# Performance work log

Measured on AMD Instinct MI355X. Metric: run time of the kernel, lower is better.

Reference implementation:

```python
import jax, jax.numpy as jnp
import numpy as np

B, S, E, A = 4, 2048, 1024, 64  # batch, seq, embedding_size, attention_size


def setup_inputs() -> dict:
    key = jax.random.key(0)
    k1, k2 = jax.random.split(key)
    embedding = jax.random.normal(k1, (B, S, E), dtype=jnp.float32)
    # nn.Linear(embedding_size, attention_size, bias=False).weight has shape [A, E]
    Wk = jax.random.normal(k2, (A, E), dtype=jnp.float32) * (1.0 / np.sqrt(E))
    return {"embedding": embedding, "Wk": Wk}


def reference(embedding, Wk):
    # NOTE: the original module (buggily) calls self.key() for q, k, AND v.
    # We reproduce that math faithfully: q = k = v = embedding @ Wk.T.
    k = jnp.einsum('bse,ae->bsa', embedding, Wk)  # [B,S,A]
    q = k
    v = k
    x = jnp.einsum('bqa,bka->bqk', q, k) / jnp.sqrt(jnp.float32(A))  # [B,S,S]
    # Faithful to masked_fill(torch.tril(x) == 0, -inf): masks the strict upper
    # triangle (tril zeros it) plus any lower-triangle entries exactly equal to 0.
    x = jnp.where(jnp.tril(x) == 0, -jnp.inf, x)
    x = jax.nn.softmax(x, axis=2)
    return jnp.einsum('bqk,bka->bqa', x, v)  # [B,S,A]
```

## Files before the change

kernel.cpp:

```cpp
#include <hip/hip_runtime.h>
#include <math.h>

#define BATCH 4
#define SLEN  2048
#define EMB   1024
#define AH    64

typedef __attribute__((ext_vector_type(8))) short bf16x8;
typedef __attribute__((ext_vector_type(4))) float f32x4;

#define MFMA16(a, b, c) __builtin_amdgcn_mfma_f32_16x16x32_bf16((a), (b), (c), 0, 0, 0)

__device__ __forceinline__ void async16(const void* g, void* l) {
  __builtin_amdgcn_global_load_lds(
      (const __attribute__((address_space(1))) unsigned int*)g,
      (__attribute__((address_space(3))) unsigned int*)l, 16, 0, 0);
}

__device__ __forceinline__ short f2bf(float x) {
  union { float f; unsigned u; } v; v.f = x;
  unsigned r = v.u + 0x7fffu + ((v.u >> 16) & 1u);
  return (short)(r >> 16);
}
__device__ __forceinline__ float bf2f(short h) {
  union { unsigned u; float f; } v; v.u = ((unsigned)(unsigned short)h) << 16;
  return v.f;
}

__device__ __forceinline__ void split_trunc(float4 a0, float4 a1, bf16x8& hi, bf16x8& lo) {
  unsigned c[8] = {__float_as_uint(a0.x), __float_as_uint(a0.y), __float_as_uint(a0.z),
                   __float_as_uint(a0.w), __float_as_uint(a1.x), __float_as_uint(a1.y),
                   __float_as_uint(a1.z), __float_as_uint(a1.w)};
  union { bf16x8 v; unsigned d[4]; } H, L;
  H.d[0] = __builtin_amdgcn_perm(c[1], c[0], 0x07060302u);
  H.d[1] = __builtin_amdgcn_perm(c[3], c[2], 0x07060302u);
  H.d[2] = __builtin_amdgcn_perm(c[5], c[4], 0x07060302u);
  H.d[3] = __builtin_amdgcn_perm(c[7], c[6], 0x07060302u);
  unsigned e[8];
#pragma unroll
  for (int j = 0; j < 8; ++j)
    e[j] = __float_as_uint(__uint_as_float(c[j]) - __uint_as_float(c[j] & 0xffff0000u));
  L.d[0] = __builtin_amdgcn_perm(e[1], e[0], 0x07060302u);
  L.d[1] = __builtin_amdgcn_perm(e[3], e[2], 0x07060302u);
  L.d[2] = __builtin_amdgcn_perm(e[5], e[4], 0x07060302u);
  L.d[3] = __builtin_amdgcn_perm(e[7], e[6], 0x07060302u);
  hi = H.v; lo = L.v;
}

__device__ __forceinline__ int slot_off(int qt) {
  return (qt == 0) ? 0 : qt + (((qt - 1) * (qt - 1)) >> 2);
}

#define CH_SHORTS 24576


__global__ __launch_bounds__(256) void prep_wk_kernel(const float* __restrict__ Wk,
                                                      short* __restrict__ BpkG) {
  int tg = blockIdx.x * 256 + threadIdx.x;
  int kc = tg >> 8, rem = tg & 255, nt = rem >> 6, lane = rem & 63;
  int n = nt * 16 + (lane & 15);
  int k = kc * 32 + (lane >> 4) * 8;
  const float* src = Wk + (size_t)n * EMB + k;
  float4 a0 = *(const float4*)src;
  float4 a1 = *(const float4*)(src + 4);
  bf16x8 hi, lo;
  split_trunc(a0, a1, hi, lo);
  short* dst = BpkG + ((size_t)(kc * 4 + nt) * 128 + lane) * 8;
  *(bf16x8*)dst = hi;
  *(bf16x8*)(dst + 512) = lo;
}

__global__ __launch_bounds__(256) void gemm_k_kernel(const float* __restrict__ emb,
                                                     const short* __restrict__ BpkG,
                                                     short* __restrict__ Kpack) {
  __shared__ __align__(16) float eT[16384];

  const int t = threadIdx.x;
  const int w = t >> 6, l = t & 63, lm = l & 15, quad = l >> 4;
  const int nt = w;
  const int row0 = blockIdx.x * 16;

  {
    int rowl = 4 * w + (l >> 4);
    int du = (l & 15) ^ (rowl & 7);
    const float* src = emb + (size_t)(row0 + rowl) * EMB + du * 4;
#pragma unroll
    for (int s = 0; s < 16; ++s)
      async16(src + s * 64, eT + s * 1024 + w * 256);
  }
  __syncthreads();

  f32x4 acc = {0.f, 0.f, 0.f, 0.f};
#pragma unroll
  for (int s = 0; s < 16; ++s) {
    const char* eS = (const char*)(eT + s * 1024);
    const short* bg = BpkG + (size_t)s * 8192;
#pragma unroll
    for (int kc = 0; kc < 2; ++kc) {
      int du0 = kc * 8 + quad * 2;
      float4 a0 = *(const float4*)(eS + lm * 256 + ((du0) ^ (lm & 7)) * 16);
      float4 a1 = *(const float4*)(eS + lm * 256 + ((du0 + 1) ^ (lm & 7)) * 16);
      bf16x8 ahi, alo;
      split_trunc(a0, a1, ahi, alo);
      bf16x8 bhi = *(const bf16x8*)(bg + (((kc * 4 + nt) * 2 + 0) * 64 + l) * 8);
      bf16x8 blo = *(const bf16x8*)(bg + (((kc * 4 + nt) * 2 + 1) * 64 + l) * 8);
      acc = MFMA16(ahi, bhi, acc);
      acc = MFMA16(ahi, blo, acc);
      acc = MFMA16(alo, bhi, acc);
    }
  }

  const int a = nt * 16 + lm;
#pragma unroll
  for (int r = 0; r < 4; ++r) {
    int srow = row0 + quad * 4 + r;
    float v = acc[r];
    short h = f2bf(v);
    short lo2 = f2bf(v - bf2f(h));
    int bb = srow >> 11, si = srow & 2047, c = si >> 7, key = si & 127;
    int kb = key >> 4, klm = key & 15;
    size_t cb = (size_t)(bb * 16 + c) * CH_SHORTS;
    size_t kbo = (size_t)((kb * 2 + (a >> 5)) * 64 + ((a & 31) >> 3) * 16 + klm) * 8 + (a & 7);
    Kpack[cb + kbo] = h;
    Kpack[cb + 8192 + kbo] = lo2;
    size_t vbo = (size_t)(((key >> 5) * 4 + (a >> 4)) * 64 + ((key & 31) >> 3) * 16 + (a & 15)) * 8 + (key & 7);
    Kpack[cb + 16384 + vbo] = h;
  }
}

__global__ __launch_bounds__(256, 4) void flash_kernel(const short* __restrict__ Kpack,
                                                       short* __restrict__ OpartH,
                                                       float2* __restrict__ mlpart) {
  const int c = blockIdx.x, qt = blockIdx.y, b = blockIdx.z;
  if (2 * c > qt) return;

  __shared__ __align__(16) short KLs[8192];
  __shared__ __align__(16) short Plds[4][16][132];

  const int t = threadIdx.x;
  const int w = t >> 6, l = t & 63, lm = l & 15, quad = l >> 4;
  const int k0 = c * 128;
  const int qr0 = qt * 64 + w * 16;

  const short* chunkG = Kpack + (size_t)(b * 16 + c) * CH_SHORTS;
#pragma unroll
  for (int u = 0; u < 4; ++u) {
    int slot = w * 4 + u;
    async16(chunkG + slot * 512 + l * 8, KLs + slot * 512);
  }

  const short* qG = Kpack + (size_t)(b * 16 + (qt >> 1)) * CH_SHORTS + ((qt & 1) * 4 + w) * 1024;
  bf16x8 qh0 = *(const bf16x8*)(qG + l * 8);
  bf16x8 qh1 = *(const bf16x8*)(qG + 512 + l * 8);
  bf16x8 ql0 = *(const bf16x8*)(qG + 8192 + l * 8);
  bf16x8 ql1 = *(const bf16x8*)(qG + 8192 + 512 + l * 8);

  bf16x8 vf[4][4];
#pragma unroll
  for (int kc2 = 0; kc2 < 4; ++kc2)
#pragma unroll
    for (int nt = 0; nt < 4; ++nt)
      vf[kc2][nt] = *(const bf16x8*)(chunkG + 16384 + ((kc2 * 4 + nt) * 64 + l) * 8);

  __syncthreads();

  f32x4 sc[8];
#pragma unroll
  for (int kg = 0; kg < 8; ++kg) {
    bf16x8 bh0 = *(const bf16x8*)(KLs + ((kg * 2 + 0) * 64 + l) * 8);
    bf16x8 bh1 = *(const bf16x8*)(KLs + ((kg * 2 + 1) * 64 + l) * 8);
    bf16x8 bl0 = *(const bf16x8*)(chunkG + 8192 + ((kg * 2 + 0) * 64 + l) * 8);
    bf16x8 bl1 = *(const bf16x8*)(chunkG + 8192 + ((kg * 2 + 1) * 64 + l) * 8);
    f32x4 s = {0.f, 0.f, 0.f, 0.f};
    s = MFMA16(qh0, bh0, s);
    s = MFMA16(qh0, bl0, s);
    s = MFMA16(ql0, bh0, s);
    s = MFMA16(qh1, bh1, s);
    s = MFMA16(qh1, bl1, s);
    s = MFMA16(ql1, bh1, s);
    sc[kg] = s;
  }

  float rm[4] = {-INFINITY, -INFINITY, -INFINITY, -INFINITY};
#pragma unroll
  for (int kg = 0; kg < 8; ++kg) {
    const int col = k0 + kg * 16 + lm;
#pragma unroll
    for (int r = 0; r < 4; ++r) {
      const int row = qr0 + quad * 4 + r;
      float v = sc[kg][r] * 0.125f;
      v = (col > row || v == 0.0f) ? -INFINITY : v;
      sc[kg][r] = v;
      rm[r] = fmaxf(rm[r], v);
    }
  }
  float m_i[4], l_i[4];
#pragma unroll
  for (int r = 0; r < 4; ++r) {
    for (int off = 1; off < 16; off <<= 1) rm[r] = fmaxf(rm[r], __shfl_xor(rm[r], off, 16));
    m_i[r] = rm[r];
  }
  float rs[4] = {0.f, 0.f, 0.f, 0.f};
#pragma unroll
  for (int kg = 0; kg < 8; ++kg)
#pragma unroll
    for (int r = 0; r < 4; ++r) {
      float p = (sc[kg][r] == -INFINITY) ? 0.f : __expf(sc[kg][r] - m_i[r]);
      sc[kg][r] = p;
      rs[r] += p;
    }
#pragma unroll
  for (int r = 0; r < 4; ++r) {
    for (int off = 1; off < 16; off <<= 1) rs[r] += __shfl_xor(rs[r], off, 16);
    l_i[r] = rs[r];
  }

#pragma unroll
  for (int kg = 0; kg < 8; ++kg)
#pragma unroll
    for (int r = 0; r < 4; ++r)
      Plds[w][quad * 4 + r][kg * 16 + lm] = f2bf(sc[kg][r]);

  f32x4 o[4] = {{0.f,0.f,0.f,0.f},{0.f,0.f,0.f,0.f},{0.f,0.f,0.f,0.f},{0.f,0.f,0.f,0.f}};
#pragma unroll
  for (int kc2 = 0; kc2 < 4; ++kc2) {
    bf16x8 pf = *(const bf16x8*)&Plds[w][lm][kc2 * 32 + quad * 8];
#pragma unroll
    for (int nt = 0; nt < 4; ++nt)
      o[nt] = MFMA16(pf, vf[kc2][nt], o[nt]);
  }

  const int slot = b * 272 + slot_off(qt) + c;
  short* Ob = OpartH + (size_t)slot * 4096;
#pragma unroll
  for (int nt = 0; nt < 4; ++nt)
#pragma unroll
    for (int r = 0; r < 4; ++r)
      Ob[(size_t)(w * 16 + quad * 4 + r) * AH + nt * 16 + lm] = f2bf(o[nt][r]);
  if (lm == 0) {
#pragma unroll
    for (int r = 0; r < 4; ++r)
      mlpart[(size_t)slot * 64 + w * 16 + quad * 4 + r] = make_float2(m_i[r], l_i[r]);
  }
}

__global__ __launch_bounds__(256) void merge_kernel(const short* __restrict__ OpartH,
                                                    const float2* __restrict__ mlpart,
                                                    float* __restrict__ out) {
  __shared__ __align__(16) short ldsO[16 * 1024];
  __shared__ float wtab[16][17];
  const int t = threadIdx.x;
  const int w = t >> 6, l = t & 63;
  const int rg = blockIdx.x, qt = blockIdx.y, b = blockIdx.z;
  const int r0 = rg * 16;
  const int nch = (qt >> 1) + 1;
  const int slotbase = b * 272 + slot_off(qt);

#pragma unroll
  for (int u = 0; u < 8; ++u) {
    int idx = w * 8 + u;
    int c = idx >> 1, half = idx & 1;
    if (c < nch)
      async16(OpartH + (size_t)(slotbase + c) * 4096 + r0 * 64 + half * 512 + l * 8,
              ldsO + c * 1024 + half * 512 + l * 8);
  }

  const int row = w * 4 + (l >> 4), c = l & 15;
  float mc = -INFINITY, lc = 0.f;
  if (c < nch) {
    float2 ml = mlpart[(size_t)(slotbase + c) * 64 + r0 + row];
    mc = ml.x; lc = ml.y;
  }
  float M = mc;
  for (int off = 1; off < 16; off <<= 1) M = fmaxf(M, __shfl_xor(M, off, 16));
  float wgt = (mc != -INFINITY) ? __expf(mc - M) : 0.f;
  float L = lc * wgt;
  for (int off = 1; off < 16; off <<= 1) L += __shfl_xor(L, off, 16);
  wtab[row][c] = wgt / L;

  __syncthreads();

  const int row2 = t >> 4, a0 = (t & 15) * 4;
  float4 acc = make_float4(0.f, 0.f, 0.f, 0.f);
  for (int cc = 0; cc < nch; ++cc) {
    float wv = wtab[row2][cc];
    short4 v4 = *(const short4*)(ldsO + cc * 1024 + row2 * 64 + a0);
    acc.x += wv * bf2f(v4.x); acc.y += wv * bf2f(v4.y);
    acc.z += wv * bf2f(v4.z); acc.w += wv * bf2f(v4.w);
  }
  *(float4*)&out[((size_t)(b * 2048 + qt * 64 + r0 + row2)) * AH + a0] = acc;
}

extern "C" void kernel_launch(void* const* d_in, const int* in_sizes, int n_in,
                              void* d_out, int out_size, void* d_ws, size_t ws_size,
                              hipStream_t stream) {
  const float* emb = (const float*)d_in[0];
  const float* Wk  = (const float*)d_in[1];
  float* out = (float*)d_out;
  char* ws = (char*)d_ws;

  short*  Kpack  = (short*)(ws);
  short*  BpkG   = (short*)(ws + 3145728);
  short*  OpartH = (short*)(ws + 3670016);
  float2* mlpart = (float2*)(ws + 12582912);

  prep_wk_kernel<<<dim3(32), dim3(256), 0, stream>>>(Wk, BpkG);
  gemm_k_kernel<<<dim3(512), dim3(256), 0, stream>>>(emb, BpkG, Kpack);
  flash_kernel<<<dim3(16, 32, 4), dim3(256), 0, stream>>>(Kpack, OpartH, mlpart);
  merge_kernel<<<dim3(4, 32, 4), dim3(256), 0, stream>>>(OpartH, mlpart, out);
}
```

Baseline: 112.4 us.

## Fuse Wk bf16 split into GEMM and stage K-low chunk in LDS

Removes the separate prep_wk kernel: gemm_k now reads fp32 Wk directly and does the hi/lo bf16 split inline, saving one launch and the packed-weight round trip. It pays for this with more global reads and redundant split work in each of the 512 blocks. Separately, the flash kernel now async-copies both the hi and lo K halves into a doubled LDS buffer instead of reading the lo half from global memory. The larger shared-memory footprint lowers the occupancy hint from 4 to 3 blocks.

```diff
diff --git a/kernel.cpp b/kernel.cpp
--- a/kernel.cpp
+++ b/kernel.cpp
@@ -54,24 +54,8 @@
 #define CH_SHORTS 24576
 
 
-__global__ __launch_bounds__(256) void prep_wk_kernel(const float* __restrict__ Wk,
-                                                      short* __restrict__ BpkG) {
-  int tg = blockIdx.x * 256 + threadIdx.x;
-  int kc = tg >> 8, rem = tg & 255, nt = rem >> 6, lane = rem & 63;
-  int n = nt * 16 + (lane & 15);
-  int k = kc * 32 + (lane >> 4) * 8;
-  const float* src = Wk + (size_t)n * EMB + k;
-  float4 a0 = *(const float4*)src;
-  float4 a1 = *(const float4*)(src + 4);
-  bf16x8 hi, lo;
-  split_trunc(a0, a1, hi, lo);
-  short* dst = BpkG + ((size_t)(kc * 4 + nt) * 128 + lane) * 8;
-  *(bf16x8*)dst = hi;
-  *(bf16x8*)(dst + 512) = lo;
-}
-
 __global__ __launch_bounds__(256) void gemm_k_kernel(const float* __restrict__ emb,
-                                                     const short* __restrict__ BpkG,
+                                                     const float* __restrict__ Wk,
                                                      short* __restrict__ Kpack) {
   __shared__ __align__(16) float eT[16384];
 
@@ -90,11 +74,12 @@
   }
   __syncthreads();
 
+  const float* wkB = Wk + (size_t)(nt * 16 + lm) * EMB + quad * 8;
+
   f32x4 acc = {0.f, 0.f, 0.f, 0.f};
 #pragma unroll
   for (int s = 0; s < 16; ++s) {
     const char* eS = (const char*)(eT + s * 1024);
-    const short* bg = BpkG + (size_t)s * 8192;
 #pragma unroll
     for (int kc = 0; kc < 2; ++kc) {
       int du0 = kc * 8 + quad * 2;
@@ -102,8 +87,11 @@
       float4 a1 = *(const float4*)(eS + lm * 256 + ((du0 + 1) ^ (lm & 7)) * 16);
       bf16x8 ahi, alo;
       split_trunc(a0, a1, ahi, alo);
-      bf16x8 bhi = *(const bf16x8*)(bg + (((kc * 4 + nt) * 2 + 0) * 64 + l) * 8);
-      bf16x8 blo = *(const bf16x8*)(bg + (((kc * 4 + nt) * 2 + 1) * 64 + l) * 8);
+      const float* bsrc = wkB + (s * 2 + kc) * 32;
+      float4 b0 = *(const float4*)(bsrc);
+      float4 b1 = *(const float4*)(bsrc + 4);
+      bf16x8 bhi, blo;
+      split_trunc(b0, b1, bhi, blo);
       acc = MFMA16(ahi, bhi, acc);
       acc = MFMA16(ahi, blo, acc);
       acc = MFMA16(alo, bhi, acc);
@@ -128,13 +116,13 @@
   }
 }
 
-__global__ __launch_bounds__(256, 4) void flash_kernel(const short* __restrict__ Kpack,
+__global__ __launch_bounds__(256, 3) void flash_kernel(const short* __restrict__ Kpack,
                                                        short* __restrict__ OpartH,
                                                        float2* __restrict__ mlpart) {
   const int c = blockIdx.x, qt = blockIdx.y, b = blockIdx.z;
   if (2 * c > qt) return;
 
-  __shared__ __align__(16) short KLs[8192];
+  __shared__ __align__(16) short KLs[16384];
   __shared__ __align__(16) short Plds[4][16][132];
 
   const int t = threadIdx.x;
@@ -144,8 +132,8 @@
 
   const short* chunkG = Kpack + (size_t)(b * 16 + c) * CH_SHORTS;
 #pragma unroll
-  for (int u = 0; u < 4; ++u) {
-    int slot = w * 4 + u;
+  for (int u = 0; u < 8; ++u) {
+    int slot = w * 8 + u;
     async16(chunkG + slot * 512 + l * 8, KLs + slot * 512);
   }
 
@@ -169,8 +157,8 @@
   for (int kg = 0; kg < 8; ++kg) {
     bf16x8 bh0 = *(const bf16x8*)(KLs + ((kg * 2 + 0) * 64 + l) * 8);
     bf16x8 bh1 = *(const bf16x8*)(KLs + ((kg * 2 + 1) * 64 + l) * 8);
-    bf16x8 bl0 = *(const bf16x8*)(chunkG + 8192 + ((kg * 2 + 0) * 64 + l) * 8);
-    bf16x8 bl1 = *(const bf16x8*)(chunkG + 8192 + ((kg * 2 + 1) * 64 + l) * 8);
+    bf16x8 bl0 = *(const bf16x8*)(KLs + 8192 + ((kg * 2 + 0) * 64 + l) * 8);
+    bf16x8 bl1 = *(const bf16x8*)(KLs + 8192 + ((kg * 2 + 1) * 64 + l) * 8);
     f32x4 s = {0.f, 0.f, 0.f, 0.f};
     s = MFMA16(qh0, bh0, s);
     s = MFMA16(qh0, bl0, s);
@@ -300,12 +288,10 @@
   char* ws = (char*)d_ws;
 
   short*  Kpack  = (short*)(ws);
-  short*  BpkG   = (short*)(ws + 3145728);
   short*  OpartH = (short*)(ws + 3670016);
   float2* mlpart = (float2*)(ws + 12582912);
 
-  prep_wk_kernel<<<dim3(32), dim3(256), 0, stream>>>(Wk, BpkG);
-  gemm_k_kernel<<<dim3(512), dim3(256), 0, stream>>>(emb, BpkG, Kpack);
+  gemm_k_kernel<<<dim3(512), dim3(256), 0, stream>>>(emb, Wk, Kpack);
   flash_kernel<<<dim3(16, 32, 4), dim3(256), 0, stream>>>(Kpack, OpartH, mlpart);
   merge_kernel<<<dim3(4, 32, 4), dim3(256), 0, stream>>>(OpartH, mlpart, out);
 }
```

Result: no change. 111.8 us (-0.6%).
